# Optimization experiments

Hardware: AMD Instinct MI355X
Metric: run time of the kernel (lower is better)

## Reference

```python
import jax, jax.numpy as jnp
import numpy as np

B, T, I, H, C = 4096, 512, 3, 32, 3  # batch, seq_len, input, hidden, classes


def setup_inputs() -> dict:
    key = jax.random.key(0)
    ks = jax.random.split(key, 7)
    s = 1.0 / np.sqrt(H)  # PyTorch LSTM init scale
    return {
        "x": jax.random.normal(ks[0], (B, T, I), dtype=jnp.float32),
        "W_ih": jax.random.normal(ks[1], (4 * H, I), dtype=jnp.float32) * s,
        "W_hh": jax.random.normal(ks[2], (4 * H, H), dtype=jnp.float32) * s,
        "b_ih": jax.random.normal(ks[3], (4 * H,), dtype=jnp.float32) * s,
        "b_hh": jax.random.normal(ks[4], (4 * H,), dtype=jnp.float32) * s,
        "W_fc": jax.random.normal(ks[5], (C, H), dtype=jnp.float32) * s,
        "b_fc": jax.random.normal(ks[6], (C,), dtype=jnp.float32) * s,
    }


def reference(x, W_ih, W_hh, b_ih, b_hh, W_fc, b_fc):
    # Precompute input contribution to all gates for every timestep: (B,T,4H)
    xg = jnp.einsum("bti,gi->btg", x, W_ih) + b_ih + b_hh
    h0 = jnp.zeros((x.shape[0], H), dtype=x.dtype)
    c0 = jnp.zeros_like(h0)

    def step(carry, xt):
        h, c = carry
        g = xt + h @ W_hh.T  # (B,4H)
        i_g, f_g, g_g, o_g = jnp.split(g, 4, axis=-1)  # PyTorch gate order i,f,g,o
        i_g = jax.nn.sigmoid(i_g)
        f_g = jax.nn.sigmoid(f_g)
        g_g = jnp.tanh(g_g)
        o_g = jax.nn.sigmoid(o_g)
        c = f_g * c + i_g * g_g
        h = o_g * jnp.tanh(c)
        return (h, c), None

    (h_last, _), _ = jax.lax.scan(step, (h0, c0), jnp.swapaxes(xg, 0, 1))
    return h_last @ W_fc.T + b_fc  # (B, num_classes)
```

## Files before the change

### kernel.cpp

```cpp
#include <hip/hip_runtime.h>
#include <cstdint>

#define B_TOT 4096
#define T_LEN 512
#define CHUNK 128
#define LOG2E 1.44269504088896340736f
#define HSTR  40

typedef _Float16 f16x8 __attribute__((ext_vector_type(8)));
typedef _Float16 f16x4 __attribute__((ext_vector_type(4)));
typedef float    f32x4 __attribute__((ext_vector_type(4)));

__device__ __forceinline__ float ex2(float v)  { return __builtin_amdgcn_exp2f(v); }
__device__ __forceinline__ float rcp_(float v) { return __builtin_amdgcn_rcpf(v); }

__global__ __launch_bounds__(512, 2)
void lstm_w8(const float* __restrict__ x,
             const float* __restrict__ W_ih,
             const float* __restrict__ W_hh,
             const float* __restrict__ b_ih,
             const float* __restrict__ b_hh,
             const float* __restrict__ W_fc,
             const float* __restrict__ b_fc,
             float* __restrict__ out)
{
    __shared__ __align__(16) _Float16 hbuf[2][16][HSTR];
    __shared__ __align__(16) _Float16 xbuf[CHUNK][16][4];

    const int tid  = threadIdx.x;
    const int wave = tid >> 6;
    const int lane = tid & 63;
    const int n    = lane & 15;
    const int kq   = lane >> 4;
    const int tb   = blockIdx.x * 16;

    const int   gate_m = n & 3;
    const int   hid_m  = 4 * wave + (n >> 2);
    const int   Rm     = gate_m * 32 + hid_m;
    const float sm     = (gate_m == 2) ? (-2.0f * LOG2E) : (-LOG2E);

    f16x8 aW;
#pragma unroll
    for (int j = 0; j < 8; ++j)
        aW[j] = (_Float16)(sm * W_hh[Rm * 32 + 8 * kq + j]);

    f16x8 a2 = {};
    if (kq == 0) {
        a2[0] = (_Float16)(sm * W_ih[Rm * 3 + 0]);
        a2[1] = (_Float16)(sm * W_ih[Rm * 3 + 1]);
        a2[2] = (_Float16)(sm * W_ih[Rm * 3 + 2]);
        a2[3] = (_Float16)(sm * (b_ih[Rm] + b_hh[Rm]));
    }

    const int hid_s = 4 * wave + kq;

    {
        int* hz = (int*)&hbuf[0][0][0];
        for (int i = tid; i < (2 * 16 * HSTR) / 2; i += 512) hz[i] = 0;
    }

    float c = 0.0f;
    f32x4 accx;

    for (int tc = 0; tc < T_LEN; tc += CHUNK) {
#pragma unroll
        for (int s = 0; s < 4; ++s) {
            const int idx = tid + s * 512;
            const int tl = idx >> 4, m = idx & 15;
            const float* xp = x + ((size_t)(tb + m) * T_LEN + (tc + tl)) * 3;
            f16x4 v;
            v[0] = (_Float16)xp[0]; v[1] = (_Float16)xp[1];
            v[2] = (_Float16)xp[2]; v[3] = (_Float16)1.0f;
            *(f16x4*)&xbuf[tl][m][0] = v;
        }
        __syncthreads();

        {
            const f16x4 xv = *(const f16x4*)&xbuf[0][n][0];
            f16x8 b2 = {};
            if (kq == 0) { b2[0] = xv[0]; b2[1] = xv[1]; b2[2] = xv[2]; b2[3] = xv[3]; }
            accx = f32x4{0.f, 0.f, 0.f, 0.f};
            accx = __builtin_amdgcn_mfma_f32_16x16x32_f16(a2, b2, accx, 0, 0, 0);
        }

#pragma unroll 2
        for (int tt = 0; tt < CHUNK; ++tt) {
            const int p = tt & 1;

            const f16x8 bh  = *(const f16x8*)&hbuf[p][n][8 * kq];
            const f32x4 acc = __builtin_amdgcn_mfma_f32_16x16x32_f16(aW, bh, accx, 0, 0, 0);

            const float iv = rcp_(1.0f + ex2(acc[0]));
            const float fv = rcp_(1.0f + ex2(acc[1]));
            const float gv = fmaf(2.0f, rcp_(1.0f + ex2(acc[2])), -1.0f);
            const float ov = rcp_(1.0f + ex2(acc[3]));

            c = fmaf(fv, c, iv * gv);
            const float th = fmaf(2.0f, rcp_(1.0f + ex2(c * (-2.0f * LOG2E))), -1.0f);
            const float h  = ov * th;

            hbuf[p ^ 1][n][hid_s] = (_Float16)h;

            const int ttn = (tt + 1 < CHUNK) ? (tt + 1) : 0;
            const f16x4 xv = *(const f16x4*)&xbuf[ttn][n][0];
            f16x8 b2 = {};
            if (kq == 0) { b2[0] = xv[0]; b2[1] = xv[1]; b2[2] = xv[2]; b2[3] = xv[3]; }
            accx = f32x4{0.f, 0.f, 0.f, 0.f};
            accx = __builtin_amdgcn_mfma_f32_16x16x32_f16(a2, b2, accx, 0, 0, 0);

            __syncthreads();
        }
    }

    if (tid < 48) {
        const int m = tid / 3, cc = tid % 3;
        float acc = b_fc[cc];
#pragma unroll
        for (int k = 0; k < 32; ++k)
            acc = fmaf(W_fc[cc * 32 + k], (float)hbuf[0][m][k], acc);
        out[(tb + m) * 3 + cc] = acc;
    }
}

extern "C" void kernel_launch(void* const* d_in, const int* in_sizes, int n_in,
                              void* d_out, int out_size, void* d_ws, size_t ws_size,
                              hipStream_t stream) {
    const float* x    = (const float*)d_in[0];
    const float* W_ih = (const float*)d_in[1];
    const float* W_hh = (const float*)d_in[2];
    const float* b_ih = (const float*)d_in[3];
    const float* b_hh = (const float*)d_in[4];
    const float* W_fc = (const float*)d_in[5];
    const float* b_fc = (const float*)d_in[6];
    float* out = (float*)d_out;

    dim3 grid(B_TOT / 16);
    dim3 block(512);
    lstm_w8<<<grid, block, 0, stream>>>(x, W_ih, W_hh, b_ih, b_hh, W_fc, b_fc, out);
}
```

Baseline: 205.6 us.

## Shrink LSTM blocks to 8 sequences with 4 waves and two MFMAs each

Each block now handles 8 batch sequences with 256 threads instead of 16 sequences with 512. Each wave issues two MFMAs per step, covering 8 hidden units, and lanes select the result half by their lane group. The intent is to cut per-step barrier cost by halving the waves that synchronise, and to double the number of blocks for better CU occupancy. The trade-off is that half of each MFMA's batch columns are redundant, so MFMA work per useful output doubles.

```diff
diff --git a/kernel.cpp b/kernel.cpp
--- a/kernel.cpp
+++ b/kernel.cpp
@@ -14,8 +14,8 @@
 __device__ __forceinline__ float ex2(float v)  { return __builtin_amdgcn_exp2f(v); }
 __device__ __forceinline__ float rcp_(float v) { return __builtin_amdgcn_rcpf(v); }
 
-__global__ __launch_bounds__(512, 2)
-void lstm_w8(const float* __restrict__ x,
+__global__ __launch_bounds__(256, 2)
+void lstm_b8(const float* __restrict__ x,
              const float* __restrict__ W_ih,
              const float* __restrict__ W_hh,
              const float* __restrict__ b_ih,
@@ -24,49 +24,53 @@
              const float* __restrict__ b_fc,
              float* __restrict__ out)
 {
-    __shared__ __align__(16) _Float16 hbuf[2][16][HSTR];
-    __shared__ __align__(16) _Float16 xbuf[CHUNK][16][4];
+    __shared__ __align__(16) _Float16 hbuf[2][8][HSTR];
+    __shared__ __align__(16) _Float16 xbuf[CHUNK][8][4];
 
     const int tid  = threadIdx.x;
     const int wave = tid >> 6;
     const int lane = tid & 63;
     const int n    = lane & 15;
     const int kq   = lane >> 4;
-    const int tb   = blockIdx.x * 16;
+    const int nb   = n & 7;
+    const int tb   = blockIdx.x * 8;
 
     const int   gate_m = n & 3;
-    const int   hid_m  = 4 * wave + (n >> 2);
-    const int   Rm     = gate_m * 32 + hid_m;
+    const int   hl_m   = n >> 2;
+    const int   R1     = gate_m * 32 + 8 * wave + hl_m;
+    const int   R2     = R1 + 4;
     const float sm     = (gate_m == 2) ? (-2.0f * LOG2E) : (-LOG2E);
 
-    f16x8 aW;
+    f16x8 aW1, aW2;
 #pragma unroll
-    for (int j = 0; j < 8; ++j)
-        aW[j] = (_Float16)(sm * W_hh[Rm * 32 + 8 * kq + j]);
-
-    f16x8 a2 = {};
+    for (int j = 0; j < 8; ++j) {
+        aW1[j] = (_Float16)(sm * W_hh[R1 * 32 + 8 * kq + j]);
+        aW2[j] = (_Float16)(sm * W_hh[R2 * 32 + 8 * kq + j]);
+    }
+    f16x8 a21 = {}, a22 = {};
     if (kq == 0) {
-        a2[0] = (_Float16)(sm * W_ih[Rm * 3 + 0]);
-        a2[1] = (_Float16)(sm * W_ih[Rm * 3 + 1]);
-        a2[2] = (_Float16)(sm * W_ih[Rm * 3 + 2]);
-        a2[3] = (_Float16)(sm * (b_ih[Rm] + b_hh[Rm]));
+        a21[0] = (_Float16)(sm * W_ih[R1 * 3 + 0]);
+        a21[1] = (_Float16)(sm * W_ih[R1 * 3 + 1]);
+        a21[2] = (_Float16)(sm * W_ih[R1 * 3 + 2]);
+        a21[3] = (_Float16)(sm * (b_ih[R1] + b_hh[R1]));
+        a22[0] = (_Float16)(sm * W_ih[R2 * 3 + 0]);
+        a22[1] = (_Float16)(sm * W_ih[R2 * 3 + 1]);
+        a22[2] = (_Float16)(sm * W_ih[R2 * 3 + 2]);
+        a22[3] = (_Float16)(sm * (b_ih[R2] + b_hh[R2]));
     }
 
-    const int hid_s = 4 * wave + kq;
+    const int hid_s = 8 * wave + kq + ((n >> 3) ? 4 : 0);
 
-    {
-        int* hz = (int*)&hbuf[0][0][0];
-        for (int i = tid; i < (2 * 16 * HSTR) / 2; i += 512) hz[i] = 0;
-    }
+    if (tid < 160) ((int*)&hbuf[0][0][0])[tid] = 0;
 
     float c = 0.0f;
-    f32x4 accx;
+    f32x4 accx1, accx2;
 
     for (int tc = 0; tc < T_LEN; tc += CHUNK) {
 #pragma unroll
         for (int s = 0; s < 4; ++s) {
-            const int idx = tid + s * 512;
-            const int tl = idx >> 4, m = idx & 15;
+            const int idx = tid + s * 256;
+            const int tl = idx >> 3, m = idx & 7;
             const float* xp = x + ((size_t)(tb + m) * T_LEN + (tc + tl)) * 3;
             f16x4 v;
             v[0] = (_Float16)xp[0]; v[1] = (_Float16)xp[1];
@@ -76,43 +80,52 @@
         __syncthreads();
 
         {
-            const f16x4 xv = *(const f16x4*)&xbuf[0][n][0];
+            const f16x4 xv = *(const f16x4*)&xbuf[0][nb][0];
             f16x8 b2 = {};
             if (kq == 0) { b2[0] = xv[0]; b2[1] = xv[1]; b2[2] = xv[2]; b2[3] = xv[3]; }
-            accx = f32x4{0.f, 0.f, 0.f, 0.f};
-            accx = __builtin_amdgcn_mfma_f32_16x16x32_f16(a2, b2, accx, 0, 0, 0);
+            const f32x4 z = {0.f, 0.f, 0.f, 0.f};
+            accx1 = __builtin_amdgcn_mfma_f32_16x16x32_f16(a21, b2, z, 0, 0, 0);
+            accx2 = __builtin_amdgcn_mfma_f32_16x16x32_f16(a22, b2, z, 0, 0, 0);
         }
 
 #pragma unroll 2
         for (int tt = 0; tt < CHUNK; ++tt) {
             const int p = tt & 1;
 
-            const f16x8 bh  = *(const f16x8*)&hbuf[p][n][8 * kq];
-            const f32x4 acc = __builtin_amdgcn_mfma_f32_16x16x32_f16(aW, bh, accx, 0, 0, 0);
+            const f16x8 bh  = *(const f16x8*)&hbuf[p][nb][8 * kq];
+            const f32x4 ac1 = __builtin_amdgcn_mfma_f32_16x16x32_f16(aW1, bh, accx1, 0, 0, 0);
+            const f32x4 ac2 = __builtin_amdgcn_mfma_f32_16x16x32_f16(aW2, bh, accx2, 0, 0, 0);
 
-            const float iv = rcp_(1.0f + ex2(acc[0]));
-            const float fv = rcp_(1.0f + ex2(acc[1]));
-            const float gv = fmaf(2.0f, rcp_(1.0f + ex2(acc[2])), -1.0f);
-            const float ov = rcp_(1.0f + ex2(acc[3]));
+            const bool hi = (n >> 3) != 0;
+            const float a0 = hi ? ac2[0] : ac1[0];
+            const float a1 = hi ? ac2[1] : ac1[1];
+            const float a2 = hi ? ac2[2] : ac1[2];
+            const float a3 = hi ? ac2[3] : ac1[3];
+
+            const float iv = rcp_(1.0f + ex2(a0));
+            const float fv = rcp_(1.0f + ex2(a1));
+            const float gv = fmaf(2.0f, rcp_(1.0f + ex2(a2)), -1.0f);
+            const float ov = rcp_(1.0f + ex2(a3));
 
             c = fmaf(fv, c, iv * gv);
             const float th = fmaf(2.0f, rcp_(1.0f + ex2(c * (-2.0f * LOG2E))), -1.0f);
             const float h  = ov * th;
 
-            hbuf[p ^ 1][n][hid_s] = (_Float16)h;
+            hbuf[p ^ 1][nb][hid_s] = (_Float16)h;
 
             const int ttn = (tt + 1 < CHUNK) ? (tt + 1) : 0;
-            const f16x4 xv = *(const f16x4*)&xbuf[ttn][n][0];
+            const f16x4 xv = *(const f16x4*)&xbuf[ttn][nb][0];
             f16x8 b2 = {};
             if (kq == 0) { b2[0] = xv[0]; b2[1] = xv[1]; b2[2] = xv[2]; b2[3] = xv[3]; }
-            accx = f32x4{0.f, 0.f, 0.f, 0.f};
-            accx = __builtin_amdgcn_mfma_f32_16x16x32_f16(a2, b2, accx, 0, 0, 0);
+            const f32x4 z = {0.f, 0.f, 0.f, 0.f};
+            accx1 = __builtin_amdgcn_mfma_f32_16x16x32_f16(a21, b2, z, 0, 0, 0);
+            accx2 = __builtin_amdgcn_mfma_f32_16x16x32_f16(a22, b2, z, 0, 0, 0);
 
             __syncthreads();
         }
     }
 
-    if (tid < 48) {
+    if (tid < 24) {
         const int m = tid / 3, cc = tid % 3;
         float acc = b_fc[cc];
 #pragma unroll
@@ -134,7 +147,7 @@
     const float* b_fc = (const float*)d_in[6];
     float* out = (float*)d_out;
 
-    dim3 grid(B_TOT / 16);
-    dim3 block(512);
-    lstm_w8<<<grid, block, 0, stream>>>(x, W_ih, W_hh, b_ih, b_hh, W_fc, b_fc, out);
+    dim3 grid(B_TOT / 8);
+    dim3 block(256);
+    lstm_b8<<<grid, block, 0, stream>>>(x, W_ih, W_hh, b_ih, b_hh, W_fc, b_fc, out);
 }
```

New measurement: 193.5 us. -5.9%, faster.

## Repartition LSTM to 4 batch rows per 2-wave block with 4 MFMAs per wave

Applied to the files above, without the earlier changes.

Each block now handles 4 batch rows with 128 threads (2 waves) instead of 16 rows with 512 threads (8 waves). Each wave issues four 16x16x32 MFMAs per step to cover 16 hidden units, and each lane selects its gate quad from the results. The intent is to cut per-step __syncthreads cost with fewer waves per block and to run 1024 smaller blocks for more parallelism. In exchange, only 4 of the 16 MFMA columns hold useful batch rows, so most MFMA work is wasted, and each wave issues more MFMAs per step.

```diff
diff --git a/kernel.cpp b/kernel.cpp
--- a/kernel.cpp
+++ b/kernel.cpp
@@ -14,8 +14,8 @@
 __device__ __forceinline__ float ex2(float v)  { return __builtin_amdgcn_exp2f(v); }
 __device__ __forceinline__ float rcp_(float v) { return __builtin_amdgcn_rcpf(v); }
 
-__global__ __launch_bounds__(512, 2)
-void lstm_w8(const float* __restrict__ x,
+__global__ __launch_bounds__(128, 2)
+void lstm_b4(const float* __restrict__ x,
              const float* __restrict__ W_ih,
              const float* __restrict__ W_hh,
              const float* __restrict__ b_ih,
@@ -24,49 +24,53 @@
              const float* __restrict__ b_fc,
              float* __restrict__ out)
 {
-    __shared__ __align__(16) _Float16 hbuf[2][16][HSTR];
-    __shared__ __align__(16) _Float16 xbuf[CHUNK][16][4];
+    __shared__ __align__(16) _Float16 hbuf[2][4][HSTR];
+    __shared__ __align__(16) _Float16 xbuf[CHUNK][4][4];
 
     const int tid  = threadIdx.x;
     const int wave = tid >> 6;
     const int lane = tid & 63;
     const int n    = lane & 15;
     const int kq   = lane >> 4;
-    const int tb   = blockIdx.x * 16;
+    const int nb   = n & 3;
+    const int tb   = blockIdx.x * 4;
 
     const int   gate_m = n & 3;
-    const int   hid_m  = 4 * wave + (n >> 2);
-    const int   Rm     = gate_m * 32 + hid_m;
+    const int   hl_m   = n >> 2;
     const float sm     = (gate_m == 2) ? (-2.0f * LOG2E) : (-LOG2E);
 
-    f16x8 aW;
+    f16x8 aW[4];
+    f16x8 a2[4];
 #pragma unroll
-    for (int j = 0; j < 8; ++j)
-        aW[j] = (_Float16)(sm * W_hh[Rm * 32 + 8 * kq + j]);
-
-    f16x8 a2 = {};
-    if (kq == 0) {
-        a2[0] = (_Float16)(sm * W_ih[Rm * 3 + 0]);
-        a2[1] = (_Float16)(sm * W_ih[Rm * 3 + 1]);
-        a2[2] = (_Float16)(sm * W_ih[Rm * 3 + 2]);
-        a2[3] = (_Float16)(sm * (b_ih[Rm] + b_hh[Rm]));
+    for (int g = 0; g < 4; ++g) {
+        const int R = gate_m * 32 + 16 * wave + 4 * g + hl_m;
+#pragma unroll
+        for (int j = 0; j < 8; ++j)
+            aW[g][j] = (_Float16)(sm * W_hh[R * 32 + 8 * kq + j]);
+        f16x8 t = {};
+        if (kq == 0) {
+            t[0] = (_Float16)(sm * W_ih[R * 3 + 0]);
+            t[1] = (_Float16)(sm * W_ih[R * 3 + 1]);
+            t[2] = (_Float16)(sm * W_ih[R * 3 + 2]);
+            t[3] = (_Float16)(sm * (b_ih[R] + b_hh[R]));
+        }
+        a2[g] = t;
     }
 
-    const int hid_s = 4 * wave + kq;
+    const int hid_s = 16 * wave + 4 * (n >> 2) + kq;
+    const int sel   = n >> 2;
 
-    {
-        int* hz = (int*)&hbuf[0][0][0];
-        for (int i = tid; i < (2 * 16 * HSTR) / 2; i += 512) hz[i] = 0;
-    }
+    if (tid < 80) ((int*)&hbuf[0][0][0])[tid] = 0;
 
     float c = 0.0f;
-    f32x4 accx;
+    const f32x4 z = {0.f, 0.f, 0.f, 0.f};
+    f32x4 accx[4];
 
     for (int tc = 0; tc < T_LEN; tc += CHUNK) {
 #pragma unroll
         for (int s = 0; s < 4; ++s) {
-            const int idx = tid + s * 512;
-            const int tl = idx >> 4, m = idx & 15;
+            const int idx = tid + s * 128;
+            const int tl = idx >> 2, m = idx & 3;
             const float* xp = x + ((size_t)(tb + m) * T_LEN + (tc + tl)) * 3;
             f16x4 v;
             v[0] = (_Float16)xp[0]; v[1] = (_Float16)xp[1];
@@ -76,43 +80,52 @@
         __syncthreads();
 
         {
-            const f16x4 xv = *(const f16x4*)&xbuf[0][n][0];
+            const f16x4 xv = *(const f16x4*)&xbuf[0][nb][0];
             f16x8 b2 = {};
             if (kq == 0) { b2[0] = xv[0]; b2[1] = xv[1]; b2[2] = xv[2]; b2[3] = xv[3]; }
-            accx = f32x4{0.f, 0.f, 0.f, 0.f};
-            accx = __builtin_amdgcn_mfma_f32_16x16x32_f16(a2, b2, accx, 0, 0, 0);
+#pragma unroll
+            for (int g = 0; g < 4; ++g)
+                accx[g] = __builtin_amdgcn_mfma_f32_16x16x32_f16(a2[g], b2, z, 0, 0, 0);
         }
 
 #pragma unroll 2
         for (int tt = 0; tt < CHUNK; ++tt) {
             const int p = tt & 1;
 
-            const f16x8 bh  = *(const f16x8*)&hbuf[p][n][8 * kq];
-            const f32x4 acc = __builtin_amdgcn_mfma_f32_16x16x32_f16(aW, bh, accx, 0, 0, 0);
+            const f16x8 bh = *(const f16x8*)&hbuf[p][nb][8 * kq];
+            f32x4 ac[4];
+#pragma unroll
+            for (int g = 0; g < 4; ++g)
+                ac[g] = __builtin_amdgcn_mfma_f32_16x16x32_f16(aW[g], bh, accx[g], 0, 0, 0);
 
-            const float iv = rcp_(1.0f + ex2(acc[0]));
-            const float fv = rcp_(1.0f + ex2(acc[1]));
-            const float gv = fmaf(2.0f, rcp_(1.0f + ex2(acc[2])), -1.0f);
-            const float ov = rcp_(1.0f + ex2(acc[3]));
+            const f32x4 lo = (sel & 2) ? ac[2] : ac[0];
+            const f32x4 hi = (sel & 2) ? ac[3] : ac[1];
+            const f32x4 q  = (sel & 1) ? hi : lo;
+
+            const float iv = rcp_(1.0f + ex2(q[0]));
+            const float fv = rcp_(1.0f + ex2(q[1]));
+            const float gv = fmaf(2.0f, rcp_(1.0f + ex2(q[2])), -1.0f);
+            const float ov = rcp_(1.0f + ex2(q[3]));
 
             c = fmaf(fv, c, iv * gv);
             const float th = fmaf(2.0f, rcp_(1.0f + ex2(c * (-2.0f * LOG2E))), -1.0f);
             const float h  = ov * th;
 
-            hbuf[p ^ 1][n][hid_s] = (_Float16)h;
+            hbuf[p ^ 1][nb][hid_s] = (_Float16)h;
 
             const int ttn = (tt + 1 < CHUNK) ? (tt + 1) : 0;
-            const f16x4 xv = *(const f16x4*)&xbuf[ttn][n][0];
+            const f16x4 xv = *(const f16x4*)&xbuf[ttn][nb][0];
             f16x8 b2 = {};
             if (kq == 0) { b2[0] = xv[0]; b2[1] = xv[1]; b2[2] = xv[2]; b2[3] = xv[3]; }
-            accx = f32x4{0.f, 0.f, 0.f, 0.f};
-            accx = __builtin_amdgcn_mfma_f32_16x16x32_f16(a2, b2, accx, 0, 0, 0);
+#pragma unroll
+            for (int g = 0; g < 4; ++g)
+                accx[g] = __builtin_amdgcn_mfma_f32_16x16x32_f16(a2[g], b2, z, 0, 0, 0);
 
             __syncthreads();
         }
     }
 
-    if (tid < 48) {
+    if (tid < 12) {
         const int m = tid / 3, cc = tid % 3;
         float acc = b_fc[cc];
 #pragma unroll
@@ -134,7 +147,7 @@
     const float* b_fc = (const float*)d_in[6];
     float* out = (float*)d_out;
 
-    dim3 grid(B_TOT / 16);
-    dim3 block(512);
-    lstm_w8<<<grid, block, 0, stream>>>(x, W_ih, W_hh, b_ih, b_hh, W_fc, b_fc, out);
+    dim3 grid(B_TOT / 4);
+    dim3 block(128);
+    lstm_b4<<<grid, block, 0, stream>>>(x, W_ih, W_hh, b_ih, b_hh, W_fc, b_fc, out);
 }
```

Result: slower. 220.1 us (+7.1%).

## Use single-wave blocks per two batch rows to drop per-step block barriers

Applied to the files above, without the earlier changes.

Replaces the 512-thread block, which handled 16 batch rows and ran a __syncthreads every timestep, with a 64-thread single-wave block that handles 2 batch rows. Each lane now computes the full gate set for its rows by issuing 8 MFMAs per step and selecting the relevant tile, so h exchange goes through LDS inside one wave with no barrier. The input projection moves from an extra MFMA to scalar FMAs on x read straight from global memory with a one-group prefetch. The cell update is also rearranged to share reciprocals. The cost is several times more MFMA work per batch row, since most columns are redundant.

```diff
diff --git a/kernel.cpp b/kernel.cpp
--- a/kernel.cpp
+++ b/kernel.cpp
@@ -3,19 +3,16 @@
 
 #define B_TOT 4096
 #define T_LEN 512
-#define CHUNK 128
 #define LOG2E 1.44269504088896340736f
-#define HSTR  40
 
 typedef _Float16 f16x8 __attribute__((ext_vector_type(8)));
-typedef _Float16 f16x4 __attribute__((ext_vector_type(4)));
 typedef float    f32x4 __attribute__((ext_vector_type(4)));
 
 __device__ __forceinline__ float ex2(float v)  { return __builtin_amdgcn_exp2f(v); }
 __device__ __forceinline__ float rcp_(float v) { return __builtin_amdgcn_rcpf(v); }
 
-__global__ __launch_bounds__(512, 2)
-void lstm_w8(const float* __restrict__ x,
+__global__ __launch_bounds__(64, 2)
+void lstm_nb(const float* __restrict__ x,
              const float* __restrict__ W_ih,
              const float* __restrict__ W_hh,
              const float* __restrict__ b_ih,
@@ -24,101 +21,111 @@
              const float* __restrict__ b_fc,
              float* __restrict__ out)
 {
-    __shared__ __align__(16) _Float16 hbuf[2][16][HSTR];
-    __shared__ __align__(16) _Float16 xbuf[CHUNK][16][4];
+    __shared__ __align__(16) _Float16 hbuf[2][32];
 
-    const int tid  = threadIdx.x;
-    const int wave = tid >> 6;
-    const int lane = tid & 63;
+    const int lane = threadIdx.x;
     const int n    = lane & 15;
     const int kq   = lane >> 4;
-    const int tb   = blockIdx.x * 16;
+    const int b    = n & 1;
+    const int v    = 4 * (n >> 1) + kq;
+    const int tb   = blockIdx.x * 2;
 
     const int   gate_m = n & 3;
-    const int   hid_m  = 4 * wave + (n >> 2);
-    const int   Rm     = gate_m * 32 + hid_m;
     const float sm     = (gate_m == 2) ? (-2.0f * LOG2E) : (-LOG2E);
-
-    f16x8 aW;
+    f16x8 aW[8];
 #pragma unroll
-    for (int j = 0; j < 8; ++j)
-        aW[j] = (_Float16)(sm * W_hh[Rm * 32 + 8 * kq + j]);
-
-    f16x8 a2 = {};
-    if (kq == 0) {
-        a2[0] = (_Float16)(sm * W_ih[Rm * 3 + 0]);
-        a2[1] = (_Float16)(sm * W_ih[Rm * 3 + 1]);
-        a2[2] = (_Float16)(sm * W_ih[Rm * 3 + 2]);
-        a2[3] = (_Float16)(sm * (b_ih[Rm] + b_hh[Rm]));
+    for (int g = 0; g < 8; ++g) {
+        const int R = gate_m * 32 + 4 * g + (n >> 2);
+#pragma unroll
+        for (int j = 0; j < 8; ++j)
+            aW[g][j] = (_Float16)(sm * W_hh[R * 32 + 8 * kq + j]);
     }
 
-    const int hid_s = 4 * wave + kq;
-
-    {
-        int* hz = (int*)&hbuf[0][0][0];
-        for (int i = tid; i < (2 * 16 * HSTR) / 2; i += 512) hz[i] = 0;
+    float wx0[4], wx1[4], wx2[4], bs[4];
+#pragma unroll
+    for (int r = 0; r < 4; ++r) {
+        const int   Rr = r * 32 + v;
+        const float sr = (r == 2) ? (-2.0f * LOG2E) : (-LOG2E);
+        wx0[r] = sr * W_ih[Rr * 3 + 0];
+        wx1[r] = sr * W_ih[Rr * 3 + 1];
+        wx2[r] = sr * W_ih[Rr * 3 + 2];
+        bs[r]  = sr * (b_ih[Rr] + b_hh[Rr]);
     }
 
+    if (lane < 32) ((int*)&hbuf[0][0])[lane] = 0;
+
+    const float4* xp = (const float4*)(x + (size_t)(tb + b) * (T_LEN * 3));
+    float4 xc0 = xp[0], xc1 = xp[1], xc2 = xp[2];
+
+    const float K2 = -2.0f * LOG2E;
     float c = 0.0f;
-    f32x4 accx;
+    const f32x4 zero = {0.f, 0.f, 0.f, 0.f};
 
-    for (int tc = 0; tc < T_LEN; tc += CHUNK) {
+    const int selb0 = (n >> 1) & 1, selb1 = (n >> 1) & 2, selb2 = (n >> 1) & 4;
+
+    for (int G = 0; G < T_LEN / 4; ++G) {
+        const int Gn = (G + 1 < T_LEN / 4) ? (G + 1) : (T_LEN / 4 - 1);
+        const float4 xn0 = xp[3 * Gn + 0];
+        const float4 xn1 = xp[3 * Gn + 1];
+        const float4 xn2 = xp[3 * Gn + 2];
+
 #pragma unroll
-        for (int s = 0; s < 4; ++s) {
-            const int idx = tid + s * 512;
-            const int tl = idx >> 4, m = idx & 15;
-            const float* xp = x + ((size_t)(tb + m) * T_LEN + (tc + tl)) * 3;
-            f16x4 v;
-            v[0] = (_Float16)xp[0]; v[1] = (_Float16)xp[1];
-            v[2] = (_Float16)xp[2]; v[3] = (_Float16)1.0f;
-            *(f16x4*)&xbuf[tl][m][0] = v;
+        for (int j = 0; j < 4; ++j) {
+            float x0, x1, x2;
+            if      (j == 0) { x0 = xc0.x; x1 = xc0.y; x2 = xc0.z; }
+            else if (j == 1) { x0 = xc0.w; x1 = xc1.x; x2 = xc1.y; }
+            else if (j == 2) { x0 = xc1.z; x1 = xc1.w; x2 = xc2.x; }
+            else             { x0 = xc2.y; x1 = xc2.z; x2 = xc2.w; }
+
+            float xq[4];
+#pragma unroll
+            for (int r = 0; r < 4; ++r)
+                xq[r] = fmaf(wx2[r], x2, fmaf(wx1[r], x1, fmaf(wx0[r], x0, bs[r])));
+
+            const f16x8 bh = *(const f16x8*)&hbuf[b][8 * kq];
+
+            f32x4 ac[8];
+#pragma unroll
+            for (int g = 0; g < 8; ++g)
+                ac[g] = __builtin_amdgcn_mfma_f32_16x16x32_f16(aW[g], bh, zero, 0, 0, 0);
+
+            const f32x4 s01 = selb0 ? ac[1] : ac[0];
+            const f32x4 s23 = selb0 ? ac[3] : ac[2];
+            const f32x4 s45 = selb0 ? ac[5] : ac[4];
+            const f32x4 s67 = selb0 ? ac[7] : ac[6];
+            const f32x4 t03 = selb1 ? s23 : s01;
+            const f32x4 t47 = selb1 ? s67 : s45;
+            const f32x4 q   = selb2 ? t47 : t03;
+
+            const float a0 = q[0] + xq[0];
+            const float a1 = q[1] + xq[1];
+            const float a2 = q[2] + xq[2];
+            const float a3 = q[3] + xq[3];
+
+            const float ei = ex2(a0), ef = ex2(a1), eg = ex2(a2), eo = ex2(a3);
+            const float pi = 1.0f + ei, pf = 1.0f + ef, pg = 1.0f + eg;
+            const float mg = 1.0f - eg;
+            const float p  = pi * pg;
+            const float qn = mg * pf;
+            const float num = fmaf(c, p, qn);
+            c = num * rcp_(pf * p);
+
+            const float ec = ex2(c * K2);
+            const float po = 1.0f + eo, pc = 1.0f + ec, mc = 1.0f - ec;
+            const float h  = mc * rcp_(po * pc);
+
+            hbuf[b][v] = (_Float16)h;
         }
-        __syncthreads();
-
-        {
-            const f16x4 xv = *(const f16x4*)&xbuf[0][n][0];
-            f16x8 b2 = {};
-            if (kq == 0) { b2[0] = xv[0]; b2[1] = xv[1]; b2[2] = xv[2]; b2[3] = xv[3]; }
-            accx = f32x4{0.f, 0.f, 0.f, 0.f};
-            accx = __builtin_amdgcn_mfma_f32_16x16x32_f16(a2, b2, accx, 0, 0, 0);
-        }
-
-#pragma unroll 2
-        for (int tt = 0; tt < CHUNK; ++tt) {
-            const int p = tt & 1;
-
-            const f16x8 bh  = *(const f16x8*)&hbuf[p][n][8 * kq];
-            const f32x4 acc = __builtin_amdgcn_mfma_f32_16x16x32_f16(aW, bh, accx, 0, 0, 0);
-
-            const float iv = rcp_(1.0f + ex2(acc[0]));
-            const float fv = rcp_(1.0f + ex2(acc[1]));
-            const float gv = fmaf(2.0f, rcp_(1.0f + ex2(acc[2])), -1.0f);
-            const float ov = rcp_(1.0f + ex2(acc[3]));
-
-            c = fmaf(fv, c, iv * gv);
-            const float th = fmaf(2.0f, rcp_(1.0f + ex2(c * (-2.0f * LOG2E))), -1.0f);
-            const float h  = ov * th;
-
-            hbuf[p ^ 1][n][hid_s] = (_Float16)h;
-
-            const int ttn = (tt + 1 < CHUNK) ? (tt + 1) : 0;
-            const f16x4 xv = *(const f16x4*)&xbuf[ttn][n][0];
-            f16x8 b2 = {};
-            if (kq == 0) { b2[0] = xv[0]; b2[1] = xv[1]; b2[2] = xv[2]; b2[3] = xv[3]; }
-            accx = f32x4{0.f, 0.f, 0.f, 0.f};
-            accx = __builtin_amdgcn_mfma_f32_16x16x32_f16(a2, b2, accx, 0, 0, 0);
-
-            __syncthreads();
-        }
+        xc0 = xn0; xc1 = xn1; xc2 = xn2;
     }
 
-    if (tid < 48) {
-        const int m = tid / 3, cc = tid % 3;
+    if (lane < 6) {
+        const int bb = lane / 3, cc = lane % 3;
         float acc = b_fc[cc];
 #pragma unroll
         for (int k = 0; k < 32; ++k)
-            acc = fmaf(W_fc[cc * 32 + k], (float)hbuf[0][m][k], acc);
-        out[(tb + m) * 3 + cc] = acc;
+            acc = fmaf(W_fc[cc * 32 + k], (float)hbuf[bb][k], acc);
+        out[(tb + bb) * 3 + cc] = acc;
     }
 }
 
@@ -134,7 +141,7 @@
     const float* b_fc = (const float*)d_in[6];
     float* out = (float*)d_out;
 
-    dim3 grid(B_TOT / 16);
-    dim3 block(512);
-    lstm_w8<<<grid, block, 0, stream>>>(x, W_ih, W_hh, b_ih, b_hh, W_fc, b_fc, out);
+    dim3 grid(B_TOT / 2);
+    dim3 block(64);
+    lstm_nb<<<grid, block, 0, stream>>>(x, W_ih, W_hh, b_ih, b_hh, W_fc, b_fc, out);
 }
```

After: 259.6 us. +26.3%, slower.
